# Kernel tuning notes

Measured on AMD Instinct MI355X. Metric: run time of the kernel, lower is better.

The kernel has to match this reference:

```python
import jax, jax.numpy as jnp
import numpy as np

K = 20  # knn neighbors (module default)


def _edge_conv(h, W, s, b):
    # h: [P, C] point features; W: [O, 2C] 1x1 conv weight; s,b: folded BN scale/shift [O]
    g = h @ h.T                                   # [P, P] inner products
    sq = jnp.sum(h * h, axis=-1)                  # [P]
    pd = 2.0 * g - sq[:, None] - sq[None, :]      # negative squared distance (torch knn)
    idx = jax.lax.top_k(pd, K)[1]                 # [P, K] nearest (includes self)
    nb = h[idx]                                   # [P, K, C]
    ctr = jnp.broadcast_to(h[:, None, :], nb.shape)
    edge = jnp.concatenate([nb - ctr, ctr], axis=-1)   # [P, K, 2C]
    y = jnp.einsum('pkc,oc->pko', edge, W)        # 1x1 conv
    y = jax.nn.leaky_relu(y * s + b, 0.2)         # BN (eval, folded) + LeakyReLU
    return jnp.max(y, axis=1)                     # max over neighbors -> [P, O]


def setup_inputs() -> dict:
    key = jax.random.key(0)
    ks = list(jax.random.split(key, 40))
    N, C, B, P = 50000, 128, 16, 1024
    d = {}
    d['features'] = jax.random.normal(ks[0], (N, C), jnp.float32)
    d['clusters'] = jax.random.randint(ks[1], (B, P), 0, N)
    i = 2
    def mk_w(shape):
        nonlocal i
        w = jax.random.normal(ks[i], shape, jnp.float32) * 0.05; i += 1
        return w
    def mk_bn(c):
        nonlocal i
        s = jax.random.uniform(ks[i], (c,), jnp.float32, 0.5, 1.5); i += 1
        b = jax.random.normal(ks[i], (c,), jnp.float32) * 0.1; i += 1
        return s, b
    # EdgeConv blocks: (out, in=2*prev)
    d['W1'] = mk_w((64, 256));  d['s1'], d['b1'] = mk_bn(64)
    d['W2'] = mk_w((64, 128));  d['s2'], d['b2'] = mk_bn(64)
    d['W3'] = mk_w((128, 128)); d['s3'], d['b3'] = mk_bn(128)
    d['W4'] = mk_w((256, 256)); d['s4'], d['b4'] = mk_bn(256)
    d['W5'] = mk_w((512, 512)); d['s5'], d['b5'] = mk_bn(512)
    d['L1'] = mk_w((512, 1024)); d['s6'], d['b6'] = mk_bn(512)
    d['L2'] = mk_w((256, 512)); d['bl2'] = jax.random.normal(ks[i], (256,), jnp.float32) * 0.05; i += 1
    d['s7'], d['b7'] = mk_bn(256)
    d['L3'] = mk_w((1, 256));   d['bl3'] = jax.random.normal(ks[i], (1,), jnp.float32) * 0.05; i += 1
    return d


def reference(clusters, features, W1, s1, b1, W2, s2, b2, W3, s3, b3,
              W4, s4, b4, W5, s5, b5, L1, s6, b6, L2, bl2, s7, b7, L3, bl3):
    def _cluster(h):  # h: [P, 128]
        x1 = _edge_conv(h,  W1, s1, b1)   # [P, 64]
        x2 = _edge_conv(x1, W2, s2, b2)   # [P, 64]
        x3 = _edge_conv(x2, W3, s3, b3)   # [P, 128]
        x4 = _edge_conv(x3, W4, s4, b4)   # [P, 256]
        xc = jnp.concatenate([x1, x2, x3, x4], axis=-1)            # [P, 512]
        y = jax.nn.leaky_relu((xc @ W5.T) * s5 + b5, 0.2)          # conv5 + BN + lrelu
        return jnp.concatenate([jnp.max(y, 0), jnp.mean(y, 0)])    # [1024] max+avg pool

    feat = jax.vmap(_cluster)(features[clusters])                  # [B, 1024]
    z = jax.nn.leaky_relu((feat @ L1.T) * s6 + b6, 0.2)            # dropout = identity (eval)
    z = jax.nn.leaky_relu((z @ L2.T + bl2) * s7 + b7, 0.2)
    z = z @ L3.T + bl3
    return jax.nn.sigmoid(z)                                       # [B, 1]
```

## Files before the change

kernel.cpp:

```cpp
#include <hip/hip_runtime.h>
#include <math.h>

#define KNN 20
#define PPTS 1024
#define NCL 16

typedef _Float16 f16x8 __attribute__((ext_vector_type(8)));
typedef _Float16 f16x4 __attribute__((ext_vector_type(4)));
typedef float f32x4 __attribute__((ext_vector_type(4)));

__device__ __forceinline__ float lrelu(float x) { return x > 0.f ? x : 0.2f * x; }

#define DPPMAX(x, ctrl) { \
    unsigned _t = (unsigned)__builtin_amdgcn_update_dpp((int)(x), (int)(x), ctrl, 0xF, 0xF, false); \
    (x) = (x) > _t ? (x) : _t; }




__global__ void gather_kernel(const float4* __restrict__ feat,
                              const int* __restrict__ clusters,
                              f16x4* __restrict__ hf,
                              float* __restrict__ sqp) {
    int n = blockIdx.x * 256 + threadIdx.x;
    int c4 = n & 31;
    int row = n >> 5;
    int src = clusters[row];
    float4 v = feat[(size_t)src * 32 + c4];
    f16x4 o;
    o[0] = (_Float16)v.x; o[1] = (_Float16)v.y; o[2] = (_Float16)v.z; o[3] = (_Float16)v.w;
    hf[(size_t)(row >> 4) * 512 + (c4 >> 3) * 128 + (row & 15) * 8 + (c4 & 7)] = o;
    float s = v.x * v.x + v.y * v.y + v.z * v.z + v.w * v.w;
    #pragma unroll
    for (int off = 16; off; off >>= 1) s += __shfl_xor(s, off);
    if (c4 == 0) { sqp[2 * row] = s; sqp[2 * row + 1] = 0.f; }
}

__global__ void tof16_tiled_kernel(const float* __restrict__ src,
                                   f16x4* __restrict__ dst) {
    int n = blockIdx.x * 256 + threadIdx.x;
    int c4 = n & 127;
    int row = n >> 7;
    float4 v = *(const float4*)&src[(size_t)row * 512 + c4 * 4];
    f16x4 o;
    o[0] = (_Float16)v.x; o[1] = (_Float16)v.y; o[2] = (_Float16)v.z; o[3] = (_Float16)v.w;
    dst[(size_t)(row >> 4) * 2048 + (c4 >> 3) * 128 + (row & 15) * 8 + (c4 & 7)] = o;
}

__global__ void wcvt_kernel(const float* __restrict__ W, int lgC4,
                            f16x4* __restrict__ wn, f16x4* __restrict__ wv) {
    int n = blockIdx.x * 256 + threadIdx.x;
    int c4 = n & ((1 << lgC4) - 1);
    int o = n >> lgC4;
    int C = 4 << lgC4;
    float4 a = *(const float4*)&W[(size_t)o * 2 * C + c4 * 4];
    float4 b = *(const float4*)&W[(size_t)o * 2 * C + C + c4 * 4];
    f16x4 on, ov;
    on[0] = (_Float16)a.x; on[1] = (_Float16)a.y; on[2] = (_Float16)a.z; on[3] = (_Float16)a.w;
    ov[0] = (_Float16)(b.x - a.x); ov[1] = (_Float16)(b.y - a.y);
    ov[2] = (_Float16)(b.z - a.z); ov[3] = (_Float16)(b.w - a.w);
    size_t ti = (size_t)(o >> 4) * (C * 4) + (c4 >> 3) * 128 + (o & 15) * 8 + (c4 & 7);
    wn[ti] = on; wv[ti] = ov;
}

template<int C>
__global__ __launch_bounds__(1024, 8) void grampk_kernel(
    const _Float16* __restrict__ hf,
    const float* __restrict__ sqp, int* __restrict__ idx)
{
    __shared__ unsigned keys[16 * 1024];
    const int f = blockIdx.x;
    const int g = f >> 3;
    const int b = (f & 7) + 8 * (g >> 6);
    const int bxi = g & 63;
    const _Float16* hb = hf + (size_t)b * PPTS * C;
    const float* sqb = sqp + 2 * (b << 10);
    const int w = threadIdx.x >> 6;
    const int lane = threadIdx.x & 63;
    const int col16 = lane & 15, quad = lane >> 4;
    const int i0 = bxi * 16;
    const int j0 = w * 64;
    const _Float16* aB = hb + (size_t)bxi * 16 * C + col16 * 32 + quad * 8;
    const _Float16* bB = hb + (size_t)(w * 4) * 16 * C + col16 * 32 + quad * 8;
    f32x4 acc[4] = {};
    #pragma unroll
    for (int kc = 0; kc < C / 32; kc++) {
        f16x8 a = *(const f16x8*)&aB[kc * 512];
        #pragma unroll
        for (int t = 0; t < 4; t++) {
            f16x8 bf = *(const f16x8*)&bB[(size_t)t * 16 * C + kc * 512];
            acc[t] = __builtin_amdgcn_mfma_f32_16x16x32_f16(a, bf, acc[t], 0, 0, 0);
        }
    }
    #pragma unroll
    for (int t = 0; t < 4; t++) {
        int j = j0 + t * 16 + col16;
        float sqj = sqb[2 * j] + sqb[2 * j + 1];
        #pragma unroll
        for (int r = 0; r < 4; r++) {
            int row = quad * 4 + r;
            float val = __builtin_fmaf(2.f, acc[t][r], -sqj);
            unsigned u = __float_as_uint(val);
            unsigned key = (u & 0x80000000u) ? ~u : (u | 0x80000000u);
            keys[(row << 10) | ((j + 2 * row) & 1023)] = (key & 0xFFFFFC00u) | (unsigned)j;
        }
    }
    __syncthreads();
    {
        const int row = w;
        const unsigned* krow = &keys[row << 10];
        unsigned m1 = 0u, m2 = 0u, m3 = 0u;
        #pragma unroll
        for (int s = 0; s < 16; s++) {
            unsigned x = krow[s * 64 + lane];
            unsigned h1 = x > m1 ? x : m1, l1 = x < m1 ? x : m1;
            unsigned h2 = l1 > m2 ? l1 : m2, l2 = l1 < m2 ? l1 : m2;
            unsigned h3 = l2 > m3 ? l2 : m3;
            m1 = h1; m2 = h2; m3 = h3;
        }
        unsigned myout = 0;
        for (int kk = 0; kk < KNN; kk++) {
            unsigned x = m1;
            DPPMAX(x, 0xB1);
            DPPMAX(x, 0x4E);
            DPPMAX(x, 0x141);
            DPPMAX(x, 0x140);
            DPPMAX(x, 0x142);
            DPPMAX(x, 0x143);
            unsigned gm = (unsigned)__builtin_amdgcn_readlane((int)x, 63);
            if (lane == kk) myout = gm & 1023u;
            if (m1 == gm) {
                if (m2 != 0u) {
                    m1 = m2; m2 = m3; m3 = 0u;
                } else {
                    unsigned n1 = 0u, n2 = 0u, n3 = 0u;
                    #pragma unroll
                    for (int s = 0; s < 16; s++) {
                        unsigned x2 = krow[s * 64 + lane];
                        x2 = x2 < gm ? x2 : 0u;
                        unsigned h1 = x2 > n1 ? x2 : n1, l1 = x2 < n1 ? x2 : n1;
                        unsigned h2 = l1 > n2 ? l1 : n2, l2 = l1 < n2 ? l1 : n2;
                        unsigned h3 = l2 > n3 ? l2 : n3;
                        n1 = h1; n2 = h2; n3 = h3;
                    }
                    m1 = n1; m2 = n2; m3 = n3;
                }
            }
        }
        if (lane < KNN) idx[((size_t)b * PPTS + i0 + row) * KNN + lane] = (int)myout;
    }
}

template<int C>
__global__ __launch_bounds__(256, 4) void uv_mfma_kernel(
    const _Float16* __restrict__ hf, int lgO,
    const _Float16* __restrict__ wn, const _Float16* __restrict__ wv,
    float* __restrict__ U, float* __restrict__ V)
{
    const int O = 1 << lgO;
    const int f = blockIdx.x;
    const int r = f >> 3;
    const int c = (f & 7) + 8 * (r >> (lgO - 2));
    const int i2 = r & ((1 << (lgO - 2)) - 1);
    const int ox = i2 & ((O >> 6) - 1);
    const int yy = i2 >> (lgO - 6);
    const int w = threadIdx.x >> 6;
    const int lane = threadIdx.x & 63;
    const int col16 = lane & 15, quad = lane >> 4;
    const int r0 = (c * 16 + yy) * 64 + w * 16;
    const int o0 = ox * 64;
    const _Float16* aB = hf + (size_t)(r0 >> 4) * 16 * C + col16 * 32 + quad * 8;
    const _Float16* nB = wn + (size_t)(o0 >> 4) * 16 * C + col16 * 32 + quad * 8;
    const _Float16* vB = wv + (size_t)(o0 >> 4) * 16 * C + col16 * 32 + quad * 8;
    f32x4 au[4] = {}, av[4] = {};
    #pragma unroll
    for (int kc = 0; kc < C / 32; kc++) {
        f16x8 a = *(const f16x8*)&aB[kc * 512];
        #pragma unroll
        for (int t = 0; t < 4; t++) {
            f16x8 bn = *(const f16x8*)&nB[(size_t)t * 16 * C + kc * 512];
            au[t] = __builtin_amdgcn_mfma_f32_16x16x32_f16(a, bn, au[t], 0, 0, 0);
            f16x8 bv = *(const f16x8*)&vB[(size_t)t * 16 * C + kc * 512];
            av[t] = __builtin_amdgcn_mfma_f32_16x16x32_f16(a, bv, av[t], 0, 0, 0);
        }
    }
    #pragma unroll
    for (int t = 0; t < 4; t++) {
        int o = o0 + t * 16 + col16;
        #pragma unroll
        for (int r2 = 0; r2 < 4; r2++) {
            int p = r0 + quad * 4 + r2;
            U[((size_t)p << lgO) + o] = au[t][r2];
            V[((size_t)p << lgO) + o] = av[t][r2];
        }
    }
}

__global__ void agg_kernel(const float* __restrict__ U, const float* __restrict__ V,
                           const int* __restrict__ idx, int lgO,
                           const float* __restrict__ sc, const float* __restrict__ bi,
                           _Float16* __restrict__ hnext,
                           _Float16* __restrict__ xcf, int co,
                           float* __restrict__ sqp)
{
    int O = 1 << lgO;
    int f = blockIdx.x;
    int rr = f >> 3;
    int c = (f & 7) + 8 * (rr >> (lgO + 2));
    int ii = rr & ((1 << (lgO + 2)) - 1);
    int n = (((c << (lgO + 2)) + ii) << 8) + threadIdx.x;
    int o = n & (O - 1);
    int pr = n >> lgO;
    int b = pr >> 10;
    const int* id = idx + (size_t)pr * KNN;
    float m = -INFINITY;
    #pragma unroll
    for (int k = 0; k < KNN; k++) {
        int j = id[k];
        float u = U[((size_t)(b * PPTS + j) << lgO) + o];
        m = fmaxf(m, u);
    }
    float val = lrelu((m + V[((size_t)pr << lgO) + o]) * sc[o] + bi[o]);
    _Float16 hv = (_Float16)val;
    int prg = pr >> 4, prr = pr & 15;
    xcf[(size_t)prg * 8192 + ((co + o) >> 5) * 512 + prr * 32 + (o & 31)] = hv;
    if (hnext) {
        hnext[(size_t)prg * 16 * O + (o >> 5) * 512 + prr * 32 + (o & 31)] = hv;
        float s = val * val;
        #pragma unroll
        for (int off = 32; off; off >>= 1) s += __shfl_xor(s, off);
        if ((threadIdx.x & 63) == 0) {
            sqp[2 * pr + ((o >> 6) & 1)] = s;
            if (lgO == 6) sqp[2 * pr + 1] = 0.f;
        }
    }
}

__global__ __launch_bounds__(256, 4) void conv5pool_kernel(
    const _Float16* __restrict__ xcf, const _Float16* __restrict__ w5f,
    const float* __restrict__ s5, const float* __restrict__ b5,
    float* __restrict__ pmax, float* __restrict__ psum)
{
    __shared__ _Float16 bsh[2][8 * 640];
    __shared__ float lmax[4][128], lsum[4][128];
    const int f = blockIdx.x;
    const int r = f >> 3;
    const int c = (f & 7) + 8 * (r >> 5);
    const int within = r & 31;
    const int pb = within >> 2;
    const int ob = within & 3;
    const int w = threadIdx.x >> 6;
    const int lane = threadIdx.x & 63;
    const int col16 = lane & 15, quad = lane >> 4;
    const int p0 = (c * 8 + pb) * 128 + w * 32;
    const int o0 = ob * 128;
    const _Float16* aB = xcf + (size_t)(p0 >> 4) * 8192 + col16 * 32 + quad * 8;
    const _Float16* bS = w5f + (size_t)(o0 >> 4) * 8192;

    auto stage = [&](int kc, int buf) {
        #pragma unroll
        for (int s = 0; s < 2; s++) {
            int h = (s * 256 + (int)threadIdx.x) * 8;
            int t = h >> 9, rr2 = (h >> 5) & 15, q = (h >> 3) & 3;
            f16x8 x = *(const f16x8*)&bS[(size_t)t * 8192 + kc * 512 + rr2 * 32 + q * 8];
            *(f16x8*)&bsh[buf][t * 640 + rr2 * 40 + q * 8] = x;
        }
    };

    stage(0, 0);
    f32x4 acc[2][8] = {};
    for (int kc = 0; kc < 16; kc++) {
        int cur = kc & 1;
        __syncthreads();
        if (kc < 15) stage(kc + 1, cur ^ 1);
        f16x8 a0 = *(const f16x8*)&aB[kc * 512];
        f16x8 a1 = *(const f16x8*)&aB[8192 + kc * 512];
        #pragma unroll
        for (int t = 0; t < 8; t++) {
            f16x8 bf = *(const f16x8*)&bsh[cur][t * 640 + col16 * 40 + quad * 8];
            acc[0][t] = __builtin_amdgcn_mfma_f32_16x16x32_f16(a0, bf, acc[0][t], 0, 0, 0);
            acc[1][t] = __builtin_amdgcn_mfma_f32_16x16x32_f16(a1, bf, acc[1][t], 0, 0, 0);
        }
    }
    #pragma unroll
    for (int t = 0; t < 8; t++) {
        int o = o0 + t * 16 + col16;
        float sc = s5[o], bi = b5[o];
        float vm = -INFINITY, vs = 0.f;
        #pragma unroll
        for (int u = 0; u < 2; u++)
            #pragma unroll
            for (int r2 = 0; r2 < 4; r2++) {
                float val = lrelu(acc[u][t][r2] * sc + bi);
                vm = fmaxf(vm, val); vs += val;
            }
        #pragma unroll
        for (int off = 16; off < 64; off <<= 1) {
            vm = fmaxf(vm, __shfl_xor(vm, off));
            vs += __shfl_xor(vs, off);
        }
        if (quad == 0) { lmax[w][t * 16 + col16] = vm; lsum[w][t * 16 + col16] = vs; }
    }
    __syncthreads();
    if (threadIdx.x < 128) {
        int col = threadIdx.x;
        float m = lmax[0][col], s = lsum[0][col];
        #pragma unroll
        for (int q = 1; q < 4; q++) { m = fmaxf(m, lmax[q][col]); s += lsum[q][col]; }
        size_t o = (size_t)(c * 8 + pb) * 512 + o0 + col;
        pmax[o] = m; psum[o] = s;
    }
}

__global__ void poolred_kernel(const float* __restrict__ pmax, const float* __restrict__ psum,
                               float* __restrict__ feat) {
    int n = blockIdx.x * 256 + threadIdx.x;
    int o = n & 511, cl = n >> 9;
    float m = -INFINITY, s = 0.f;
    #pragma unroll
    for (int c = 0; c < 8; c++) {
        size_t q = (size_t)(cl * 8 + c) * 512 + o;
        m = fmaxf(m, pmax[q]); s += psum[q];
    }
    feat[(size_t)cl * 1024 + o] = m;
    feat[(size_t)cl * 1024 + 512 + o] = s * (1.f / 1024.f);
}

__global__ void mlp1_kernel(const float* __restrict__ feat, const float* __restrict__ L1,
                            const float* __restrict__ s6, const float* __restrict__ b6,
                            float* __restrict__ z1) {
    int wid = (blockIdx.x * 256 + threadIdx.x) >> 6;
    int lane = threadIdx.x & 63;
    int o = wid & 511, b = wid >> 9;
    const float* f = feat + (size_t)b * 1024;
    const float* w = L1 + (size_t)o * 1024;
    float acc = 0.f;
    #pragma unroll
    for (int i = 0; i < 16; i++) acc = fmaf(f[i * 64 + lane], w[i * 64 + lane], acc);
    #pragma unroll
    for (int off = 32; off; off >>= 1) acc += __shfl_xor(acc, off);
    if (lane == 0) z1[wid] = lrelu(acc * s6[o] + b6[o]);
}

__global__ void mlp2_kernel(const float* __restrict__ z1, const float* __restrict__ L2,
                            const float* __restrict__ bl2,
                            const float* __restrict__ s7, const float* __restrict__ b7,
                            float* __restrict__ z2) {
    int wid = (blockIdx.x * 256 + threadIdx.x) >> 6;
    int lane = threadIdx.x & 63;
    int o = wid & 255, b = wid >> 8;
    const float* f = z1 + (size_t)b * 512;
    const float* w = L2 + (size_t)o * 512;
    float acc = 0.f;
    #pragma unroll
    for (int i = 0; i < 8; i++) acc = fmaf(f[i * 64 + lane], w[i * 64 + lane], acc);
    #pragma unroll
    for (int off = 32; off; off >>= 1) acc += __shfl_xor(acc, off);
    if (lane == 0) z2[wid] = lrelu((acc + bl2[o]) * s7[o] + b7[o]);
}

__global__ void mlp3_kernel(const float* __restrict__ z2, const float* __restrict__ L3,
                            const float* __restrict__ bl3, float* __restrict__ out) {
    __shared__ float red[256];
    int t = threadIdx.x;
    int b = t >> 4, q = t & 15;
    float acc = 0.f;
    for (int c = q * 16; c < q * 16 + 16; c++) acc = fmaf(z2[(size_t)b * 256 + c], L3[c], acc);
    red[t] = acc;
    __syncthreads();
    if (q == 0) {
        float s = 0.f;
        #pragma unroll
        for (int i = 0; i < 16; i++) s += red[b * 16 + i];
        s += bl3[0];
        out[b] = 1.f / (1.f + expf(-s));
    }
}

extern "C" void kernel_launch(void* const* d_in, const int* in_sizes, int n_in,
                              void* d_out, int out_size, void* d_ws, size_t ws_size,
                              hipStream_t stream) {
    const float* features = (const float*)d_in[0];
    const int*   clusters = (const int*)d_in[1];
    const float* W1 = (const float*)d_in[2];
    const float* s1 = (const float*)d_in[3];
    const float* b1 = (const float*)d_in[4];
    const float* W2 = (const float*)d_in[5];
    const float* s2 = (const float*)d_in[6];
    const float* b2 = (const float*)d_in[7];
    const float* W3 = (const float*)d_in[8];
    const float* s3 = (const float*)d_in[9];
    const float* b3 = (const float*)d_in[10];
    const float* W4 = (const float*)d_in[11];
    const float* s4 = (const float*)d_in[12];
    const float* b4 = (const float*)d_in[13];
    const float* W5 = (const float*)d_in[14];
    const float* s5 = (const float*)d_in[15];
    const float* b5 = (const float*)d_in[16];
    const float* L1 = (const float*)d_in[17];
    const float* s6 = (const float*)d_in[18];
    const float* b6 = (const float*)d_in[19];
    const float* L2 = (const float*)d_in[20];
    const float* bl2 = (const float*)d_in[21];
    const float* s7 = (const float*)d_in[22];
    const float* b7 = (const float*)d_in[23];
    const float* L3 = (const float*)d_in[24];
    const float* bl3 = (const float*)d_in[25];

    float* ws = (float*)d_ws;
    float* U   = ws;
    float* V   = U + 4194304;
    _Float16* xcf16 = (_Float16*)(V + 4194304);
    _Float16* w5f16 = xcf16 + 8388608;
    _Float16* hf16  = w5f16 + 262144;
    _Float16* wn16  = hf16 + 2097152;
    _Float16* wv16  = wn16 + 32768;
    int*   idx  = (int*)(wv16 + 32768);
    float* sqp  = (float*)(idx + 327680);
    float* pmax = sqp + 32768;
    float* psum = pmax + 131072;
    float* feat = psum + 131072;
    float* z1   = feat + 16384;
    float* z2   = z1 + 8192;

    gather_kernel<<<2048, 256, 0, stream>>>((const float4*)features, clusters,
                                            (f16x4*)hf16, sqp);

    auto stage = [&](int C, int O, int lgO,
                     const float* W, const float* sc, const float* bi,
                     int co, _Float16* hnext) {
        int lgC4 = (C == 128) ? 5 : 4;
        if (C == 128)
            grampk_kernel<128><<<1024, 1024, 0, stream>>>(hf16, sqp, idx);
        else
            grampk_kernel<64><<<1024, 1024, 0, stream>>>(hf16, sqp, idx);
        wcvt_kernel<<<(O * (C / 4)) / 256, 256, 0, stream>>>(W, lgC4, (f16x4*)wn16, (f16x4*)wv16);
        if (C == 128)
            uv_mfma_kernel<128><<<(O >> 6) * 256, 256, 0, stream>>>(hf16, lgO, wn16, wv16, U, V);
        else
            uv_mfma_kernel<64><<<(O >> 6) * 256, 256, 0, stream>>>(hf16, lgO, wn16, wv16, U, V);
        agg_kernel<<<(NCL * PPTS * O) / 256, 256, 0, stream>>>(U, V, idx, lgO, sc, bi,
                                                               hnext, xcf16, co, sqp);
    };

    stage(128,  64, 6, W1, s1, b1, 0,   hf16);
    stage( 64,  64, 6, W2, s2, b2, 64,  hf16);
    stage( 64, 128, 7, W3, s3, b3, 128, hf16);
    stage(128, 256, 8, W4, s4, b4, 256, (_Float16*)nullptr);

    tof16_tiled_kernel<<<256, 256, 0, stream>>>(W5, (f16x4*)w5f16);
    conv5pool_kernel<<<512, 256, 0, stream>>>(xcf16, w5f16, s5, b5, pmax, psum);
    poolred_kernel<<<32, 256, 0, stream>>>(pmax, psum, feat);
    mlp1_kernel<<<2048, 256, 0, stream>>>(feat, L1, s6, b6, z1);
    mlp2_kernel<<<1024, 256, 0, stream>>>(z1, L2, bl2, s7, b7, z2);
    mlp3_kernel<<<1, 256, 0, stream>>>(z2, L3, bl3, (float*)d_out);
}
```

Measured before the change: 356.3 us.

## Replace shared-memory key matrix with in-register sorted top-k and two-stage merge

The gram/top-k kernel now swaps operand roles so each lane holds 16 candidate keys for one query row in registers. It bitonic-sorts them and extracts a per-wave top-20 with cross-quad shuffles. These partial lists go into a much smaller shared buffer, and a second stage merges 320 candidates per row with sorted per-lane lists of 5. This removes the 64KB LDS key matrix and the rescanning fallback, and should raise occupancy. The cost is more register pressure, and launch bounds are lowered to 4.

```diff
diff --git a/kernel.cpp b/kernel.cpp
--- a/kernel.cpp
+++ b/kernel.cpp
@@ -64,11 +64,11 @@
 }
 
 template<int C>
-__global__ __launch_bounds__(1024, 8) void grampk_kernel(
+__global__ __launch_bounds__(1024, 4) void grampk_kernel(
     const _Float16* __restrict__ hf,
     const float* __restrict__ sqp, int* __restrict__ idx)
 {
-    __shared__ unsigned keys[16 * 1024];
+    __shared__ unsigned st[16 * 16 * 20];
     const int f = blockIdx.x;
     const int g = f >> 3;
     const int b = (f & 7) + 8 * (g >> 6);
@@ -79,48 +79,77 @@
     const int lane = threadIdx.x & 63;
     const int col16 = lane & 15, quad = lane >> 4;
     const int i0 = bxi * 16;
-    const int j0 = w * 64;
-    const _Float16* aB = hb + (size_t)bxi * 16 * C + col16 * 32 + quad * 8;
-    const _Float16* bB = hb + (size_t)(w * 4) * 16 * C + col16 * 32 + quad * 8;
+    const _Float16* aB = hb + (size_t)(w * 4) * 16 * C + col16 * 32 + quad * 8;
+    const _Float16* bB = hb + (size_t)bxi * 16 * C + col16 * 32 + quad * 8;
     f32x4 acc[4] = {};
     #pragma unroll
     for (int kc = 0; kc < C / 32; kc++) {
-        f16x8 a = *(const f16x8*)&aB[kc * 512];
+        f16x8 bfrag = *(const f16x8*)&bB[kc * 512];
         #pragma unroll
         for (int t = 0; t < 4; t++) {
-            f16x8 bf = *(const f16x8*)&bB[(size_t)t * 16 * C + kc * 512];
-            acc[t] = __builtin_amdgcn_mfma_f32_16x16x32_f16(a, bf, acc[t], 0, 0, 0);
-        }
-    }
+            f16x8 afrag = *(const f16x8*)&aB[(size_t)t * 16 * C + kc * 512];
+            acc[t] = __builtin_amdgcn_mfma_f32_16x16x32_f16(afrag, bfrag, acc[t], 0, 0, 0);
+        }
+    }
+    float sqv = sqb[2 * (w * 64 + lane)] + sqb[2 * (w * 64 + lane) + 1];
+    unsigned key[16];
     #pragma unroll
     for (int t = 0; t < 4; t++) {
-        int j = j0 + t * 16 + col16;
-        float sqj = sqb[2 * j] + sqb[2 * j + 1];
         #pragma unroll
         for (int r = 0; r < 4; r++) {
-            int row = quad * 4 + r;
+            int jl = t * 16 + quad * 4 + r;
+            float sqj = __shfl(sqv, jl, 64);
             float val = __builtin_fmaf(2.f, acc[t][r], -sqj);
             unsigned u = __float_as_uint(val);
-            unsigned key = (u & 0x80000000u) ? ~u : (u | 0x80000000u);
-            keys[(row << 10) | ((j + 2 * row) & 1023)] = (key & 0xFFFFFC00u) | (unsigned)j;
-        }
+            unsigned k2 = (u & 0x80000000u) ? ~u : (u | 0x80000000u);
+            key[t * 4 + r] = (k2 & 0xFFFFFC00u) | (unsigned)(w * 64 + jl);
+        }
+    }
+    #pragma unroll
+    for (int p = 1; p < 16; p <<= 1)
+        #pragma unroll
+        for (int k2 = p; k2 >= 1; k2 >>= 1)
+            #pragma unroll
+            for (int j2 = k2 & (p - 1); j2 + k2 < 16; j2 += 2 * k2)
+                #pragma unroll
+                for (int i2 = 0; i2 < k2; i2++)
+                    if ((i2 + j2 + k2 < 16) && ((i2 + j2) / (2 * p) == (i2 + j2 + k2) / (2 * p))) {
+                        unsigned a = key[i2 + j2], c2 = key[i2 + j2 + k2];
+                        key[i2 + j2] = a > c2 ? a : c2;
+                        key[i2 + j2 + k2] = a > c2 ? c2 : a;
+                    }
+    #pragma unroll
+    for (int kk = 0; kk < KNN; kk++) {
+        unsigned x = key[0];
+        unsigned y = (unsigned)__shfl_xor((int)x, 16);  x = x > y ? x : y;
+        y = (unsigned)__shfl_xor((int)x, 32);           x = x > y ? x : y;
+        if (quad == (kk & 3)) st[w * 320 + col16 * 20 + kk] = x;
+        bool wl = (key[0] == x);
+        #pragma unroll
+        for (int s = 0; s < 15; s++) key[s] = wl ? key[s + 1] : key[s];
+        key[15] = wl ? 0u : key[15];
     }
     __syncthreads();
     {
-        const int row = w;
-        const unsigned* krow = &keys[row << 10];
-        unsigned m1 = 0u, m2 = 0u, m3 = 0u;
-        #pragma unroll
-        for (int s = 0; s < 16; s++) {
-            unsigned x = krow[s * 64 + lane];
-            unsigned h1 = x > m1 ? x : m1, l1 = x < m1 ? x : m1;
-            unsigned h2 = l1 > m2 ? l1 : m2, l2 = l1 < m2 ? l1 : m2;
-            unsigned h3 = l2 > m3 ? l2 : m3;
-            m1 = h1; m2 = h2; m3 = h3;
+        unsigned cand[5];
+        #pragma unroll
+        for (int s = 0; s < 5; s++) {
+            int flat = lane * 5 + s;
+            cand[s] = st[(flat / 20) * 320 + w * 20 + (flat % 20)];
+        }
+        #pragma unroll
+        for (int rnd = 0; rnd < 5; rnd++) {
+            #pragma unroll
+            for (int s = rnd & 1; s + 1 < 5; s += 2) {
+                unsigned a = cand[s], c2 = cand[s + 1];
+                cand[s] = a > c2 ? a : c2;
+                cand[s + 1] = a > c2 ? c2 : a;
+            }
         }
         unsigned myout = 0;
+        #pragma unroll
         for (int kk = 0; kk < KNN; kk++) {
-            unsigned x = m1;
+            unsigned x = cand[0];
             DPPMAX(x, 0xB1);
             DPPMAX(x, 0x4E);
             DPPMAX(x, 0x141);
@@ -129,25 +158,12 @@
             DPPMAX(x, 0x143);
             unsigned gm = (unsigned)__builtin_amdgcn_readlane((int)x, 63);
             if (lane == kk) myout = gm & 1023u;
-            if (m1 == gm) {
-                if (m2 != 0u) {
-                    m1 = m2; m2 = m3; m3 = 0u;
-                } else {
-                    unsigned n1 = 0u, n2 = 0u, n3 = 0u;
-                    #pragma unroll
-                    for (int s = 0; s < 16; s++) {
-                        unsigned x2 = krow[s * 64 + lane];
-                        x2 = x2 < gm ? x2 : 0u;
-                        unsigned h1 = x2 > n1 ? x2 : n1, l1 = x2 < n1 ? x2 : n1;
-                        unsigned h2 = l1 > n2 ? l1 : n2, l2 = l1 < n2 ? l1 : n2;
-                        unsigned h3 = l2 > n3 ? l2 : n3;
-                        n1 = h1; n2 = h2; n3 = h3;
-                    }
-                    m1 = n1; m2 = n2; m3 = n3;
-                }
-            }
-        }
-        if (lane < KNN) idx[((size_t)b * PPTS + i0 + row) * KNN + lane] = (int)myout;
+            bool wl = (cand[0] == gm);
+            #pragma unroll
+            for (int s = 0; s < 4; s++) cand[s] = wl ? cand[s + 1] : cand[s];
+            cand[4] = wl ? 0u : cand[4];
+        }
+        if (lane < KNN) idx[((size_t)b * PPTS + i0 + w) * KNN + lane] = (int)myout;
     }
 }
 
```

New measurement: 376.9 us. +5.8%, slower.
